# Optimization experiments

Measured on AMD Instinct MI355X. Metric: run time of the kernel, lower is better.

Reference implementation:

```python
import jax, jax.numpy as jnp
import numpy as np

N_NODES = 100000
N_EDGES = 3200000
N_GRAPHS = 1000
FEAT = 512
EMB = 7
N_CLASSES = 10


def gcn_conv(x, W, b, src, dst, n_nodes):
    # PyG GCNConv: add self-loops, symmetric normalization, aggregate src->dst.
    h = x @ W  # [N, emb] — transform first (emb is tiny)
    loops = jnp.arange(n_nodes, dtype=src.dtype)
    es = jnp.concatenate([src, loops])
    ed = jnp.concatenate([dst, loops])
    deg = jax.ops.segment_sum(jnp.ones_like(ed, dtype=h.dtype), ed, num_segments=n_nodes)
    dinv = jnp.where(deg > 0, jax.lax.rsqrt(deg), 0.0)
    norm = dinv[es] * dinv[ed]  # [E+N]
    msgs = h[es] * norm[:, None]
    out = jax.ops.segment_sum(msgs, ed, num_segments=n_nodes)
    return out + b


def setup_inputs() -> dict:
    key = jax.random.key(0)
    ks = jax.random.split(key, 8)
    x = jax.random.normal(ks[0], (N_NODES, FEAT), dtype=jnp.float32)
    edge_index = jax.random.randint(ks[1], (2, N_EDGES), 0, N_NODES, dtype=jnp.int64)
    batch_index = jnp.sort(jax.random.randint(ks[2], (N_NODES,), 0, N_GRAPHS, dtype=jnp.int64))
    s_in = 1.0 / np.sqrt(FEAT)
    s_h = 1.0 / np.sqrt(EMB)
    W_in = jax.random.uniform(ks[3], (FEAT, EMB), jnp.float32, -s_in, s_in)
    b_in = jnp.zeros((EMB,), jnp.float32)
    W_conv1 = jax.random.uniform(ks[4], (EMB, EMB), jnp.float32, -s_h, s_h)
    b_conv1 = jnp.zeros((EMB,), jnp.float32)
    W_out = jax.random.uniform(ks[5], (EMB, N_CLASSES), jnp.float32, -s_h, s_h)
    b_out = jax.random.uniform(ks[6], (N_CLASSES,), jnp.float32, -s_h, s_h)
    return {"x": x, "edge_index": edge_index, "batch_index": batch_index,
            "W_in": W_in, "b_in": b_in, "W_conv1": W_conv1, "b_conv1": b_conv1,
            "W_out": W_out, "b_out": b_out}


def reference(x, edge_index, batch_index, W_in, b_in, W_conv1, b_conv1, W_out, b_out):
    src, dst = edge_index[0], edge_index[1]
    out = jax.nn.relu(gcn_conv(x, W_in, b_in, src, dst, N_NODES))  # [N, 7]
    # final_conv_acts (computed by the original but NOT used in the returned logits)
    _final_conv_acts = jax.nn.relu(gcn_conv(out, W_conv1, b_conv1, src, dst, N_NODES))
    # global mean pool over batch_index (on `out`, matching the original forward)
    sums = jax.ops.segment_sum(out, batch_index, num_segments=N_GRAPHS)
    counts = jax.ops.segment_sum(jnp.ones((N_NODES,), out.dtype), batch_index, num_segments=N_GRAPHS)
    pooled = sums / jnp.maximum(counts, 1.0)[:, None]  # [G, 7]
    logits = pooled @ W_out + b_out  # [G, classes]
    return jax.nn.softmax(logits, axis=1)
```

## Files before the change

kernel.cpp:

```cpp
#include <hip/hip_runtime.h>

#define N_NODES   100000
#define N_EDGES   3200000
#define N_GRAPHS  1000
#define FEAT      512
#define EMB       7
#define HP        8
#define N_CLASSES 10

#define BSH       8
#define DMASK     255
#define NBUCK     391
#define TCOLS     392
#define NB_A      512
#define TILE_A    6250
#define SEGCAP    9216
#define MMF       391

__device__ __forceinline__ int load_idx(const void* p, long long i, int is32) {
    if (is32) return ((const int*)p)[i];
    return (int)((const long long*)p)[i];
}

__device__ int edge_is32(const void* p) {
    __shared__ int sflag;
    if (threadIdx.x == 0) sflag = 0;
    __syncthreads();
    const int* w = (const int*)p;
    int any = 0;
    for (int k = threadIdx.x; k < 2048; k += blockDim.x)
        if (w[2 * k + 1] != 0) any = 1;
    if (any) atomicOr(&sflag, 1);
    __syncthreads();
    return sflag;
}

__device__ int batch_is32(const void* p) {
    __shared__ int sflag;
    if (threadIdx.x == 0) sflag = 0;
    __syncthreads();
    const int* w = (const int*)p;
    int any = 0;
    for (int k = 1024 + threadIdx.x; k < 2048; k += blockDim.x)
        if (w[2 * k + 1] != 0) any = 1;
    if (any) atomicOr(&sflag, 1);
    __syncthreads();
    return sflag;
}

__device__ void mm_span(int nbase, const float* __restrict__ x,
                        const float* __restrict__ W, float* __restrict__ h) {
    int n = nbase + (int)threadIdx.x;
    if (n >= N_NODES) return;
    const float4* xr = (const float4*)(x + (size_t)n * FEAT);
    float acc[EMB];
#pragma unroll
    for (int j = 0; j < EMB; ++j) acc[j] = 0.0f;
#pragma unroll 4
    for (int k4 = 0; k4 < FEAT / 4; ++k4) {
        float4 v = xr[k4];
        const float* w = W + k4 * 4 * EMB;
#pragma unroll
        for (int j = 0; j < EMB; ++j) {
            float a = acc[j];
            a = fmaf(v.x, w[0 * EMB + j], a);
            a = fmaf(v.y, w[1 * EMB + j], a);
            a = fmaf(v.z, w[2 * EMB + j], a);
            a = fmaf(v.w, w[3 * EMB + j], a);
            acc[j] = a;
        }
    }
    float4* o = (float4*)(h + (size_t)n * HP);
    o[0] = make_float4(acc[0], acc[1], acc[2], acc[3]);
    o[1] = make_float4(acc[4], acc[5], acc[6], 0.0f);
}

__global__ void k_sortblk(const void* __restrict__ eidx, int* __restrict__ T,
                          int* __restrict__ gpk, const float* __restrict__ x,
                          const float* __restrict__ W, float* __restrict__ h) {
    if (blockIdx.x >= NB_A) { mm_span(((int)blockIdx.x - NB_A) * 256, x, W, h); return; }
    __shared__ int stage[TILE_A];
    __shared__ int bins[NBUCK];
    __shared__ int cur[NBUCK];
    __shared__ int pairv[256];
    __shared__ int wsum[4];
    int is32 = edge_is32(eidx);
    const int b = (int)blockIdx.x, t = (int)threadIdx.x;
    for (int k = t; k < NBUCK; k += 256) bins[k] = 0;
    __syncthreads();
    long long e0 = (long long)b * TILE_A;
    for (int i = t; i < TILE_A; i += 256) {
        int d = load_idx(eidx, (long long)N_EDGES + e0 + i, is32);
        atomicAdd(&bins[d >> BSH], 1);
    }
    __syncthreads();
    int c0 = (2 * t     < NBUCK) ? bins[2 * t]     : 0;
    int c1 = (2 * t + 1 < NBUCK) ? bins[2 * t + 1] : 0;
    int pr = c0 + c1;
    int inc = pr;
    for (int o = 1; o < 64; o <<= 1) {
        int u = __shfl_up(inc, o);
        if ((t & 63) >= o) inc += u;
    }
    if ((t & 63) == 63) wsum[t >> 6] = inc;
    pairv[t] = inc;
    __syncthreads();
    int add = 0, wv = t >> 6;
    if (wv >= 1) add += wsum[0];
    if (wv >= 2) add += wsum[1];
    if (wv >= 3) add += wsum[2];
    int excl = inc + add - pr;
    __syncthreads();
    if (2 * t     < NBUCK) { bins[2 * t]     = excl;      cur[2 * t]     = excl; }
    if (2 * t + 1 < NBUCK) { bins[2 * t + 1] = excl + c0; cur[2 * t + 1] = excl + c0; }
    __syncthreads();
    for (int k = t; k < NBUCK; k += 256)
        T[b * TCOLS + k] = b * TILE_A + bins[k];
    if (t == 0) T[b * TCOLS + NBUCK] = (b + 1) * TILE_A;
    for (int i = t; i < TILE_A; i += 256) {
        int src = load_idx(eidx, e0 + i, is32);
        int d   = load_idx(eidx, (long long)N_EDGES + e0 + i, is32);
        int slot = atomicAdd(&cur[d >> BSH], 1);
        stage[slot] = src | ((d & DMASK) << 17);
    }
    __syncthreads();
    for (int i = t; i < TILE_A; i += 256)
        gpk[b * TILE_A + i] = stage[i];
}

__device__ int load_runs(const int* __restrict__ T, int k,
                         int* rstart, int* rst, int* pairv, int* wsum) {
    const int t = (int)threadIdx.x;
    int b0 = 2 * t, b1 = 2 * t + 1;
    int s0 = T[b0 * TCOLS + k], e0 = T[b0 * TCOLS + k + 1];
    int s1 = T[b1 * TCOLS + k], e1 = T[b1 * TCOLS + k + 1];
    rstart[b0] = s0; rstart[b1] = s1;
    int c0 = e0 - s0, c1 = e1 - s1;
    int pr = c0 + c1;
    int inc = pr;
    for (int o = 1; o < 64; o <<= 1) {
        int u = __shfl_up(inc, o);
        if ((t & 63) >= o) inc += u;
    }
    if ((t & 63) == 63) wsum[t >> 6] = inc;
    __syncthreads();
    int add = 0, wv = t >> 6;
    if (wv >= 1) add += wsum[0];
    if (wv >= 2) add += wsum[1];
    if (wv >= 3) add += wsum[2];
    int excl = inc + add - pr;
    rst[b0] = excl;
    rst[b1] = excl + c0;
    if (t == 255) rst[512] = excl + pr;
    __syncthreads();
    return rst[512];
}

__device__ __forceinline__ int run_of(const int* rst, int i) {
    int lo = 0, hi = 512;
    while (lo + 1 < hi) { int m = (lo + hi) >> 1; if (rst[m] <= i) lo = m; else hi = m; }
    return lo;
}

__global__ void k_nodecnt(const int* __restrict__ T, const int* __restrict__ gpk,
                          int* __restrict__ cnt, float* __restrict__ h) {
    __shared__ int rstart[512], rst[513], pairv[256], wsum[4];
    __shared__ int bin[256];
    const int k = (int)blockIdx.x, t = (int)threadIdx.x;
    bin[t] = 0;
    int total = load_runs(T, k, rstart, rst, pairv, wsum);
    __syncthreads();
    for (int i = t; i < total; i += 256) {
        int b = run_of(rst, i);
        int p = gpk[rstart[b] + (i - rst[b])];
        atomicAdd(&bin[(p >> 17) & DMASK], 1);
    }
    __syncthreads();
    int node = (k << BSH) + t;
    if (node < N_NODES) {
        int c = bin[t];
        cnt[node] = c;
        float di = rsqrtf((float)c + 1.0f);
        float4* hp = (float4*)(h + (size_t)node * HP);
        float4 a = hp[0], cc = hp[1];
        hp[0] = make_float4(a.x * di, a.y * di, a.z * di, a.w * di);
        hp[1] = make_float4(cc.x * di, cc.y * di, cc.z * di, 0.0f);
    }
}

__global__ void k_ggather(const int* __restrict__ T, const int* __restrict__ gpk,
                          const int* __restrict__ cnt, const float* __restrict__ h,
                          const float* __restrict__ b_in, float* __restrict__ outn) {
    __shared__ int stage[SEGCAP];
    __shared__ int rstart[512], rst[513], pairv[256], wsum[4];
    __shared__ int bin[256], loff[256], curs[256];
    const int k = (int)blockIdx.x, t = (int)threadIdx.x;
    int total = load_runs(T, k, rstart, rst, pairv, wsum);
    int len = (total > SEGCAP) ? SEGCAP : total;
    {
        int node = (k << BSH) + t;
        bin[t] = (node < N_NODES) ? cnt[node] : 0;
        curs[t] = 0;
    }
    __syncthreads();
    {
        int v = bin[t];
        int inc = v;
        for (int o = 1; o < 64; o <<= 1) {
            int u = __shfl_up(inc, o);
            if ((t & 63) >= o) inc += u;
        }
        pairv[t] = inc;
        __syncthreads();
        int add = 0, wv = t >> 6;
        if (wv >= 1) add += pairv[63];
        if (wv >= 2) add += pairv[127];
        if (wv >= 3) add += pairv[191];
        loff[t] = inc + add - v;
    }
    __syncthreads();
    for (int i = t; i < len; i += 256) {
        int b = run_of(rst, i);
        int p = gpk[rstart[b] + (i - rst[b])];
        int dl = (p >> 17) & DMASK;
        int r = atomicAdd(&curs[dl], 1);
        stage[loff[dl] + r] = p & 0x1FFFF;
    }
    __syncthreads();
    const float4* h4 = (const float4*)h;
    int q = t & 3;
#pragma unroll
    for (int g4 = 0; g4 < 4; ++g4) {
        int nl = (t >> 2) + g4 * 64;
        int node = (k << BSH) + nl;
        if (node < N_NODES) {
            int o = loff[nl], c = bin[nl];
            float acc[EMB];
#pragma unroll
            for (int j = 0; j < EMB; ++j) acc[j] = 0.0f;
            for (int kk = q; kk < c; kk += 4) {
                int s = stage[o + kk];
                float4 a4 = h4[(size_t)s * 2];
                float4 c4 = h4[(size_t)s * 2 + 1];
                acc[0] += a4.x; acc[1] += a4.y; acc[2] += a4.z; acc[3] += a4.w;
                acc[4] += c4.x; acc[5] += c4.y; acc[6] += c4.z;
            }
            if (q == 0) {
                float4 a4 = h4[(size_t)node * 2];
                float4 c4 = h4[(size_t)node * 2 + 1];
                acc[0] += a4.x; acc[1] += a4.y; acc[2] += a4.z; acc[3] += a4.w;
                acc[4] += c4.x; acc[5] += c4.y; acc[6] += c4.z;
            }
#pragma unroll
            for (int j = 0; j < EMB; ++j) {
                acc[j] += __shfl_xor(acc[j], 1);
                acc[j] += __shfl_xor(acc[j], 2);
            }
            float di = rsqrtf((float)c + 1.0f);
            int j0 = 2 * q;
            float v0 = fmaxf(fmaf(di, acc[j0], b_in[j0]), 0.0f);
            float v1 = (j0 + 1 < EMB)
                     ? fmaxf(fmaf(di, acc[j0 + 1], b_in[j0 + 1]), 0.0f) : 0.0f;
            ((float2*)(outn + (size_t)node * HP))[q] = make_float2(v0, v1);
        }
    }
}

__global__ void k_pool(const float* __restrict__ outn, const void* __restrict__ batch,
                       const float* __restrict__ W_out, const float* __restrict__ b_out,
                       float* __restrict__ out) {
    int g = blockIdx.x;
    int is32 = batch_is32(batch);
    int n0, n1;
    {
        int lo = 0, hi = N_NODES;
        while (lo < hi) { int m = (lo + hi) >> 1; if (load_idx(batch, m, is32) < g) lo = m + 1; else hi = m; }
        n0 = lo;
        hi = N_NODES;
        while (lo < hi) { int m = (lo + hi) >> 1; if (load_idx(batch, m, is32) < g + 1) lo = m + 1; else hi = m; }
        n1 = lo;
    }
    float acc[EMB];
#pragma unroll
    for (int j = 0; j < EMB; ++j) acc[j] = 0.0f;
    for (int n = n0 + (int)threadIdx.x; n < n1; n += (int)blockDim.x) {
        const float4* o4 = (const float4*)(outn + (size_t)n * HP);
        float4 a = o4[0], b = o4[1];
        acc[0] += a.x; acc[1] += a.y; acc[2] += a.z; acc[3] += a.w;
        acc[4] += b.x; acc[5] += b.y; acc[6] += b.z;
    }
#pragma unroll
    for (int j = 0; j < EMB; ++j) {
        float v = acc[j];
        for (int o = 32; o > 0; o >>= 1) v += __shfl_down(v, o);
        acc[j] = v;
    }
    __shared__ float sred[4][EMB];
    int wave = threadIdx.x >> 6, lane = threadIdx.x & 63;
    if (lane == 0) {
#pragma unroll
        for (int j = 0; j < EMB; ++j) sred[wave][j] = acc[j];
    }
    __syncthreads();
    if (threadIdx.x == 0) {
        float sums[EMB];
#pragma unroll
        for (int j = 0; j < EMB; ++j)
            sums[j] = sred[0][j] + sred[1][j] + sred[2][j] + sred[3][j];
        float inv = 1.0f / fmaxf((float)(n1 - n0), 1.0f);
        float logit[N_CLASSES];
        float mx = -1e30f;
#pragma unroll
        for (int c = 0; c < N_CLASSES; ++c) {
            float l = b_out[c];
#pragma unroll
            for (int j = 0; j < EMB; ++j)
                l = fmaf(sums[j] * inv, W_out[j * N_CLASSES + c], l);
            logit[c] = l;
            mx = fmaxf(mx, l);
        }
        float se = 0.0f;
#pragma unroll
        for (int c = 0; c < N_CLASSES; ++c) {
            logit[c] = expf(logit[c] - mx);
            se += logit[c];
        }
        float is = 1.0f / se;
#pragma unroll
        for (int c = 0; c < N_CLASSES; ++c)
            out[(size_t)g * N_CLASSES + c] = logit[c] * is;
    }
}

extern "C" void kernel_launch(void* const* d_in, const int* in_sizes, int n_in,
                              void* d_out, int out_size, void* d_ws, size_t ws_size,
                              hipStream_t stream) {
    const float* x     = (const float*)d_in[0];
    const void*  eidx  = d_in[1];
    const void*  batch = d_in[2];
    const float* W_in  = (const float*)d_in[3];
    const float* b_in  = (const float*)d_in[4];
    const float* W_out = (const float*)d_in[7];
    const float* b_out = (const float*)d_in[8];
    float* out = (float*)d_out;

    int*   gpk  = (int*)d_ws;
    int*   T    = gpk + N_EDGES;
    int*   cnt  = T + NB_A * TCOLS;
    float* h    = (float*)(cnt + N_NODES);
    float* outn = h + (size_t)N_NODES * HP;

    const int B = 256;
    k_sortblk<<<NB_A + MMF, B, 0, stream>>>(eidx, T, gpk, x, W_in, h);
    k_nodecnt<<<NBUCK, B, 0, stream>>>(T, gpk, cnt, h);
    k_ggather<<<NBUCK, B, 0, stream>>>(T, gpk, cnt, h, b_in, outn);
    k_pool   <<<N_GRAPHS, B, 0, stream>>>(outn, batch, W_out, b_out, out);
}
```

Baseline: 164.0 us.

## Fuse mean-pool accumulation into gather kernel and cache edge tiles in registers

The gather kernel now accumulates each node's ReLU output straight into per-graph sums. It uses a shared-memory window of graphs and falls back to global atomics when a graph lies outside the window. This drops the outn buffer and the per-graph pooling pass, and a small per-graph kernel then computes the logits and softmax. Separately, the block sort keeps each packed edge and its bucket in registers from the counting pass, so the edge indices are not read a second time. The costs are float atomics, which make the summation order nondeterministic, and higher register pressure from the unrolled 25-element arrays.

```diff
diff --git a/kernel.cpp b/kernel.cpp
--- a/kernel.cpp
+++ b/kernel.cpp
@@ -14,8 +14,10 @@
 #define TCOLS     392
 #define NB_A      512
 #define TILE_A    6250
+#define NIT       25
 #define SEGCAP    9216
 #define MMF       391
+#define GSPAN     16
 
 __device__ __forceinline__ int load_idx(const void* p, long long i, int is32) {
     if (is32) return ((const int*)p)[i];
@@ -89,9 +91,17 @@
     for (int k = t; k < NBUCK; k += 256) bins[k] = 0;
     __syncthreads();
     long long e0 = (long long)b * TILE_A;
-    for (int i = t; i < TILE_A; i += 256) {
-        int d = load_idx(eidx, (long long)N_EDGES + e0 + i, is32);
-        atomicAdd(&bins[d >> BSH], 1);
+    int pk[NIT], bk[NIT];
+#pragma unroll
+    for (int it = 0; it < NIT; ++it) {
+        int i = it * 256 + t;
+        if (i < TILE_A) {
+            int src = load_idx(eidx, e0 + i, is32);
+            int d   = load_idx(eidx, (long long)N_EDGES + e0 + i, is32);
+            pk[it] = src | ((d & DMASK) << 17);
+            bk[it] = d >> BSH;
+            atomicAdd(&bins[bk[it]], 1);
+        } else { pk[it] = 0; bk[it] = -1; }
     }
     __syncthreads();
     int c0 = (2 * t     < NBUCK) ? bins[2 * t]     : 0;
@@ -117,11 +127,12 @@
     for (int k = t; k < NBUCK; k += 256)
         T[b * TCOLS + k] = b * TILE_A + bins[k];
     if (t == 0) T[b * TCOLS + NBUCK] = (b + 1) * TILE_A;
-    for (int i = t; i < TILE_A; i += 256) {
-        int src = load_idx(eidx, e0 + i, is32);
-        int d   = load_idx(eidx, (long long)N_EDGES + e0 + i, is32);
-        int slot = atomicAdd(&cur[d >> BSH], 1);
-        stage[slot] = src | ((d & DMASK) << 17);
+#pragma unroll
+    for (int it = 0; it < NIT; ++it) {
+        if (bk[it] >= 0) {
+            int slot = atomicAdd(&cur[bk[it]], 1);
+            stage[slot] = pk[it];
+        }
     }
     __syncthreads();
     for (int i = t; i < TILE_A; i += 256)
@@ -129,7 +140,7 @@
 }
 
 __device__ int load_runs(const int* __restrict__ T, int k,
-                         int* rstart, int* rst, int* pairv, int* wsum) {
+                         int* rstart, int* rst, int* wsum) {
     const int t = (int)threadIdx.x;
     int b0 = 2 * t, b1 = 2 * t + 1;
     int s0 = T[b0 * TCOLS + k], e0 = T[b0 * TCOLS + k + 1];
@@ -163,12 +174,17 @@
 }
 
 __global__ void k_nodecnt(const int* __restrict__ T, const int* __restrict__ gpk,
-                          int* __restrict__ cnt, float* __restrict__ h) {
-    __shared__ int rstart[512], rst[513], pairv[256], wsum[4];
+                          int* __restrict__ cnt, float* __restrict__ h,
+                          float* __restrict__ gsum) {
+    __shared__ int rstart[512], rst[513], wsum[4];
     __shared__ int bin[256];
     const int k = (int)blockIdx.x, t = (int)threadIdx.x;
+    if (k < 32) {
+        int idx = k * 256 + t;
+        if (idx < N_GRAPHS * 8) gsum[idx] = 0.0f;
+    }
     bin[t] = 0;
-    int total = load_runs(T, k, rstart, rst, pairv, wsum);
+    int total = load_runs(T, k, rstart, rst, wsum);
     __syncthreads();
     for (int i = t; i < total; i += 256) {
         int b = run_of(rst, i);
@@ -190,12 +206,18 @@
 
 __global__ void k_ggather(const int* __restrict__ T, const int* __restrict__ gpk,
                           const int* __restrict__ cnt, const float* __restrict__ h,
-                          const float* __restrict__ b_in, float* __restrict__ outn) {
+                          const float* __restrict__ b_in, const void* __restrict__ batch,
+                          float* __restrict__ gsum) {
     __shared__ int stage[SEGCAP];
-    __shared__ int rstart[512], rst[513], pairv[256], wsum[4];
-    __shared__ int bin[256], loff[256], curs[256];
+    __shared__ int rstart[512], rst[513], wsum[4];
+    __shared__ int bin[256], loff[256], curs[256], pairv[256];
+    __shared__ float gsl[GSPAN][8];
+    __shared__ int gmin_s;
     const int k = (int)blockIdx.x, t = (int)threadIdx.x;
-    int total = load_runs(T, k, rstart, rst, pairv, wsum);
+    int bis32 = batch_is32(batch);
+    if (t == 0) gmin_s = load_idx(batch, (long long)(k << BSH), bis32);
+    if (t < GSPAN * 8) ((float*)gsl)[t] = 0.0f;
+    int total = load_runs(T, k, rstart, rst, wsum);
     int len = (total > SEGCAP) ? SEGCAP : total;
     {
         int node = (k << BSH) + t;
@@ -203,6 +225,7 @@
         curs[t] = 0;
     }
     __syncthreads();
+    const int gmin = gmin_s;
     {
         int v = bin[t];
         int inc = v;
@@ -261,16 +284,32 @@
             float v0 = fmaxf(fmaf(di, acc[j0], b_in[j0]), 0.0f);
             float v1 = (j0 + 1 < EMB)
                      ? fmaxf(fmaf(di, acc[j0 + 1], b_in[j0 + 1]), 0.0f) : 0.0f;
-            ((float2*)(outn + (size_t)node * HP))[q] = make_float2(v0, v1);
+            int g = load_idx(batch, node, bis32);
+            int gi = g - gmin;
+            if (gi < GSPAN) {
+                atomicAdd(&gsl[gi][j0], v0);
+                atomicAdd(&gsl[gi][j0 + 1], v1);
+            } else {
+                atomicAdd(&gsum[(size_t)g * 8 + j0], v0);
+                atomicAdd(&gsum[(size_t)g * 8 + j0 + 1], v1);
+            }
         }
     }
-}
-
-__global__ void k_pool(const float* __restrict__ outn, const void* __restrict__ batch,
-                       const float* __restrict__ W_out, const float* __restrict__ b_out,
-                       float* __restrict__ out) {
-    int g = blockIdx.x;
+    __syncthreads();
+    if (t < GSPAN * 8) {
+        int r = t >> 3, c = t & 7;
+        float v = gsl[r][c];
+        int g = gmin + r;
+        if (v != 0.0f && g < N_GRAPHS) atomicAdd(&gsum[(size_t)g * 8 + c], v);
+    }
+}
+
+__global__ void k_final(const float* __restrict__ gsum, const void* __restrict__ batch,
+                        const float* __restrict__ W_out, const float* __restrict__ b_out,
+                        float* __restrict__ out) {
     int is32 = batch_is32(batch);
+    int g = (int)blockIdx.x * 256 + (int)threadIdx.x;
+    if (g >= N_GRAPHS) return;
     int n0, n1;
     {
         int lo = 0, hi = N_NODES;
@@ -280,56 +319,31 @@
         while (lo < hi) { int m = (lo + hi) >> 1; if (load_idx(batch, m, is32) < g + 1) lo = m + 1; else hi = m; }
         n1 = lo;
     }
-    float acc[EMB];
-#pragma unroll
-    for (int j = 0; j < EMB; ++j) acc[j] = 0.0f;
-    for (int n = n0 + (int)threadIdx.x; n < n1; n += (int)blockDim.x) {
-        const float4* o4 = (const float4*)(outn + (size_t)n * HP);
-        float4 a = o4[0], b = o4[1];
-        acc[0] += a.x; acc[1] += a.y; acc[2] += a.z; acc[3] += a.w;
-        acc[4] += b.x; acc[5] += b.y; acc[6] += b.z;
-    }
-#pragma unroll
-    for (int j = 0; j < EMB; ++j) {
-        float v = acc[j];
-        for (int o = 32; o > 0; o >>= 1) v += __shfl_down(v, o);
-        acc[j] = v;
-    }
-    __shared__ float sred[4][EMB];
-    int wave = threadIdx.x >> 6, lane = threadIdx.x & 63;
-    if (lane == 0) {
-#pragma unroll
-        for (int j = 0; j < EMB; ++j) sred[wave][j] = acc[j];
-    }
-    __syncthreads();
-    if (threadIdx.x == 0) {
-        float sums[EMB];
+    float inv = 1.0f / fmaxf((float)(n1 - n0), 1.0f);
+    float sums[EMB];
+#pragma unroll
+    for (int j = 0; j < EMB; ++j) sums[j] = gsum[(size_t)g * 8 + j] * inv;
+    float logit[N_CLASSES];
+    float mx = -1e30f;
+#pragma unroll
+    for (int c = 0; c < N_CLASSES; ++c) {
+        float l = b_out[c];
 #pragma unroll
         for (int j = 0; j < EMB; ++j)
-            sums[j] = sred[0][j] + sred[1][j] + sred[2][j] + sred[3][j];
-        float inv = 1.0f / fmaxf((float)(n1 - n0), 1.0f);
-        float logit[N_CLASSES];
-        float mx = -1e30f;
-#pragma unroll
-        for (int c = 0; c < N_CLASSES; ++c) {
-            float l = b_out[c];
-#pragma unroll
-            for (int j = 0; j < EMB; ++j)
-                l = fmaf(sums[j] * inv, W_out[j * N_CLASSES + c], l);
-            logit[c] = l;
-            mx = fmaxf(mx, l);
-        }
-        float se = 0.0f;
-#pragma unroll
-        for (int c = 0; c < N_CLASSES; ++c) {
-            logit[c] = expf(logit[c] - mx);
-            se += logit[c];
-        }
-        float is = 1.0f / se;
-#pragma unroll
-        for (int c = 0; c < N_CLASSES; ++c)
-            out[(size_t)g * N_CLASSES + c] = logit[c] * is;
-    }
+            l = fmaf(sums[j], W_out[j * N_CLASSES + c], l);
+        logit[c] = l;
+        mx = fmaxf(mx, l);
+    }
+    float se = 0.0f;
+#pragma unroll
+    for (int c = 0; c < N_CLASSES; ++c) {
+        logit[c] = expf(logit[c] - mx);
+        se += logit[c];
+    }
+    float is = 1.0f / se;
+#pragma unroll
+    for (int c = 0; c < N_CLASSES; ++c)
+        out[(size_t)g * N_CLASSES + c] = logit[c] * is;
 }
 
 extern "C" void kernel_launch(void* const* d_in, const int* in_sizes, int n_in,
@@ -348,11 +362,11 @@
     int*   T    = gpk + N_EDGES;
     int*   cnt  = T + NB_A * TCOLS;
     float* h    = (float*)(cnt + N_NODES);
-    float* outn = h + (size_t)N_NODES * HP;
+    float* gsum = h + (size_t)N_NODES * HP;
 
     const int B = 256;
     k_sortblk<<<NB_A + MMF, B, 0, stream>>>(eidx, T, gpk, x, W_in, h);
-    k_nodecnt<<<NBUCK, B, 0, stream>>>(T, gpk, cnt, h);
-    k_ggather<<<NBUCK, B, 0, stream>>>(T, gpk, cnt, h, b_in, outn);
-    k_pool   <<<N_GRAPHS, B, 0, stream>>>(outn, batch, W_out, b_out, out);
-}
+    k_nodecnt<<<NBUCK, B, 0, stream>>>(T, gpk, cnt, h, gsum);
+    k_ggather<<<NBUCK, B, 0, stream>>>(T, gpk, cnt, h, b_in, batch, gsum);
+    k_final  <<<(N_GRAPHS + B - 1) / B, B, 0, stream>>>(gsum, batch, W_out, b_out, out);
+}
```

After: 165.0 us. About the same (+0.6%).
